# Optimization experiments

Measured on AMD Instinct MI355X. Metric: run time of the kernel, lower is better.

The kernel has to match this reference:

```python
import jax, jax.numpy as jnp
import numpy as np

LAYERS = 3
N_NODES = 100000
N_EDGES = 800000
EMB = 100
EPS = 1e-12  # F.normalize default eps


def setup_inputs() -> dict:
    key = jax.random.key(0)
    ks = jax.random.split(key, 7)
    embedding = jax.random.normal(ks[0], (N_NODES, EMB), dtype=jnp.float32)
    adj_val = jax.random.uniform(ks[1], (N_EDGES,), dtype=jnp.float32)
    w_att = jax.random.normal(ks[2], (EMB, 1), dtype=jnp.float32) * 0.1
    b_att = jax.random.normal(ks[3], (1,), dtype=jnp.float32) * 0.1
    w_items = jax.random.normal(ks[4], (LAYERS, EMB, EMB), dtype=jnp.float32) * 0.1
    adj_row = jax.random.randint(ks[5], (N_EDGES,), 0, N_NODES, dtype=jnp.int32)
    adj_col = jax.random.randint(ks[6], (N_EDGES,), 0, N_NODES, dtype=jnp.int32)
    return {"embedding": embedding, "adj_val": adj_val, "w_att": w_att,
            "b_att": b_att, "w_items": w_items, "adj_row": adj_row, "adj_col": adj_col}


def reference(embedding, adj_val, w_att, b_att, w_items, adj_row, adj_col):
    n = embedding.shape[0]
    # column-degree normalization: adjacency.multiply(1/adjacency.sum(axis=0))
    degree = jax.ops.segment_sum(adj_val, adj_col, num_segments=n)  # [N]
    vals = adj_val / degree[adj_col]  # per-edge normalized value

    x = embedding
    final = embedding
    for i in range(LAYERS):
        scores = x @ w_att + b_att              # [N,1]
        attw = jax.nn.softmax(scores, axis=0)   # softmax over nodes (dim=0)
        x = x @ w_items[i].T                    # nn.Linear (no bias)
        m = x * attw                            # attention-weighted features
        # sparse mm: out[r] = sum_{edges e: row[e]=r} vals[e] * m[col[e]]
        gathered = m[adj_col] * vals[:, None]   # [E, EMB]
        x = jax.ops.segment_sum(gathered, adj_row, num_segments=n)
        # F.normalize(p=2, dim=-1)
        norm = jnp.linalg.norm(x, axis=-1, keepdims=True)
        x = x / jnp.maximum(norm, EPS)
        final = final + x
    return final / (LAYERS + 1)
```

## Files before the change

### kernel.cpp

```cpp
#include <hip/hip_runtime.h>
#include <hip/hip_bf16.h>

#define NN 100000
#define NE 800000
#define EM 100
#define NL 3

typedef short bf16x8 __attribute__((ext_vector_type(8)));
typedef float f32x4  __attribute__((ext_vector_type(4)));

static constexpr size_t OFF_XB   = 0;
static constexpr size_t OFF_M    = OFF_XB   + (size_t)NN*128*2;
static constexpr size_t OFF_F    = OFF_M    + (size_t)NN*128*2;
static constexpr size_t OFF_DEG  = OFF_F    + (size_t)NN*EM*2;
static constexpr size_t OFF_SC   = OFF_DEG  + (size_t)NN*4;
static constexpr size_t OFF_ES   = OFF_SC   + (size_t)NN*4;
static constexpr size_t OFF_CNT  = OFF_ES   + (size_t)NE*8;
static constexpr size_t OFF_RP   = OFF_CNT  + (size_t)NN*4;
static constexpr size_t OFF_CUR  = OFF_RP   + (size_t)(NN+64)*4;
static constexpr size_t OFF_BS   = OFF_CUR  + (size_t)NN*4;
static constexpr size_t OFF_BIN  = OFF_BS   + 512;
static constexpr size_t OFF_FLAG = OFF_BIN  + 16384;
static constexpr size_t OFF_WAT  = OFF_FLAG + 16;
static constexpr size_t OFF_WBF  = OFF_WAT  + 512;

__device__ inline float ldf(const void* p, int i, int f32) {
    return f32 ? ((const float*)p)[i]
               : __bfloat162float(((const __hip_bfloat16*)p)[i]);
}

__device__ inline float bflo(unsigned int u) { return __uint_as_float(u << 16); }
__device__ inline float bfhi(unsigned int u) { return __uint_as_float(u & 0xFFFF0000u); }
__device__ inline unsigned int pack2bf(float a, float b) {
    __hip_bfloat16 ha = __float2bfloat16(a), hb = __float2bfloat16(b);
    unsigned short ua = *(unsigned short*)&ha, ub = *(unsigned short*)&hb;
    return (unsigned int)ua | ((unsigned int)ub << 16);
}

__device__ inline int probe_block(const void* p, int nsamp) {
    __shared__ int sflag;
    int tid = threadIdx.x;
    if (tid < 64) {
        const unsigned short* h = (const unsigned short*)p;
        int big = 0;
        for (int i = tid; i < nsamp; i += 64) {
            int ex = (h[2 * i] >> 7) & 0xFF;
            big += (ex >= 134) ? 1 : 0;
        }
        #pragma unroll
        for (int off = 32; off; off >>= 1) big += __shfl_xor(big, off);
        if (tid == 0) sflag = (big >= 2) ? 1 : 0;
    }
    __syncthreads();
    int f = sflag;
    __syncthreads();
    return f;
}

__global__ __launch_bounds__(256) void k_setup(const void* w_att, const void* w_itm,
                                               float* deg, int* counts, float* bins,
                                               float* wat, unsigned short* wbf) {
    int fw = probe_block(w_att, 50);
    int fi = probe_block(w_itm, 256);
    int i = blockIdx.x * 256 + threadIdx.x;
    if (i < NN) { deg[i] = 0.f; counts[i] = 0; }
    if (i < 4096) bins[i] = 0.f;
    if (i < 128) wat[i] = (i < EM) ? ldf(w_att, i, fw) : 0.f;
    if (i < NL * 112 * 128) {
        int l = i / (112 * 128), rem = i % (112 * 128);
        int n = rem >> 7, k = rem & 127;
        float v = (n < EM && k < EM) ? ldf(w_itm, (l * EM + n) * EM + k, fi) : 0.f;
        __hip_bfloat16 b = __float2bfloat16(v);
        wbf[i] = *(unsigned short*)&b;
    }
}

__global__ __launch_bounds__(256) void k_initxf(const void* __restrict__ emb,
                                                const float* __restrict__ wat,
                                                unsigned int* __restrict__ xbf,
                                                unsigned int* __restrict__ fin,
                                                float* __restrict__ scores, int* flags,
                                                float* __restrict__ bins) {
    __shared__ float sb[4];
    int femb = probe_block(emb, 256);
    if (blockIdx.x == 0 && threadIdx.x == 0) flags[0] = femb;
    int lane = threadIdx.x & 63, w = threadIdx.x >> 6;
    int r = blockIdx.x * 4 + w;
    float f0 = 0.f, f1 = 0.f, part = 0.f;
    bool act = lane < 50;
    if (act) {
        if (femb) {
            float2 t = ((const float2*)emb)[(size_t)r * 50 + lane];
            f0 = t.x; f1 = t.y;
        } else {
            unsigned int u = ((const unsigned int*)emb)[(size_t)r * 50 + lane];
            f0 = bflo(u); f1 = bfhi(u);
        }
        float2 wv = *(const float2*)(wat + 2 * lane);
        part = f0 * wv.x + f1 * wv.y;
        fin[(size_t)r * 50 + lane] = pack2bf(f0, f1);
    }
    xbf[(size_t)r * 64 + lane] = act ? pack2bf(f0, f1) : 0u;
    #pragma unroll
    for (int off = 32; off; off >>= 1) part += __shfl_xor(part, off);
    if (lane == 0) {
        float p = expf(part);
        scores[r] = p;
        sb[w] = p;
    }
    __syncthreads();
    if (threadIdx.x == 0)
        atomicAdd(&bins[blockIdx.x & 1023], sb[0] + sb[1] + sb[2] + sb[3]);
}

__global__ __launch_bounds__(256) void k_deg(const void* __restrict__ val,
                                             const int* __restrict__ row, const int* __restrict__ col,
                                             float* deg, int* counts) {
    int fav = probe_block(val, 256);
    int e = blockIdx.x * 256 + threadIdx.x;
    if (e >= NE) return;
    atomicAdd(&deg[col[e]], ldf(val, e, fav));
    atomicAdd(&counts[row[e]], 1);
}

__global__ __launch_bounds__(256) void k_scanA(const int* __restrict__ counts, int* excl, int* bsum) {
    __shared__ int s[256];
    int base = blockIdx.x * 1024;
    int tid = threadIdx.x;
    int v[4]; int t = 0;
    #pragma unroll
    for (int i = 0; i < 4; i++) {
        int idx = base + tid * 4 + i;
        v[i] = (idx < NN) ? counts[idx] : 0;
        t += v[i];
    }
    s[tid] = t; __syncthreads();
    for (int off = 1; off < 256; off <<= 1) {
        int add = (tid >= off) ? s[tid - off] : 0;
        __syncthreads();
        s[tid] += add;
        __syncthreads();
    }
    int ex = (tid == 0) ? 0 : s[tid - 1];
    #pragma unroll
    for (int i = 0; i < 4; i++) {
        int idx = base + tid * 4 + i;
        if (idx < NN) excl[idx] = ex;
        ex += v[i];
    }
    if (tid == 255) bsum[blockIdx.x] = s[255];
}

__global__ __launch_bounds__(256) void k_scanC(int* rowptr, int* cursor, const int* __restrict__ bsum) {
    __shared__ int spfx;
    int tid = threadIdx.x;
    int gi = blockIdx.x >> 2;
    if (tid < 64) {
        int t = (tid < gi) ? bsum[tid] : 0;
        if (tid + 64 < gi) t += bsum[tid + 64];
        #pragma unroll
        for (int off = 32; off; off >>= 1) t += __shfl_xor(t, off);
        if (tid == 0) spfx = t;
    }
    __syncthreads();
    int pfx = spfx;
    int i = blockIdx.x * 256 + tid;
    if (i < NN) {
        int v = rowptr[i] + pfx;
        rowptr[i] = v; cursor[i] = v;
        if (i == 0) rowptr[NN] = NE;
    }
}

__global__ __launch_bounds__(256) void k_scatter(const int* __restrict__ row, const int* __restrict__ col,
                                                 const void* __restrict__ aval,
                                                 const float* __restrict__ deg, int* cursor,
                                                 int2* es) {
    int fav = probe_block(aval, 256);
    int e = blockIdx.x * 256 + threadIdx.x;
    if (e >= NE) return;
    int r = row[e];
    int c = col[e];
    int pos = atomicAdd(&cursor[r], 1);
    float v = ldf(aval, e, fav) / deg[c];
    es[pos] = make_int2(c, __float_as_int(v));
}

__global__ __launch_bounds__(256) void k_gemm(const unsigned short* __restrict__ xbf,
                                              const unsigned short* __restrict__ wbf,
                                              const float* __restrict__ scores,
                                              const float* __restrict__ bins,
                                              unsigned short* __restrict__ m, int layer) {
    int wid = threadIdx.x >> 6, lane = threadIdx.x & 63;
    int row0 = blockIdx.x * 64 + wid * 16;
    if (row0 >= NN) return;
    int c15 = lane & 15, quad = lane >> 4;

    float bsum = 0.f;
    const f32x4* bp = (const f32x4*)(bins + layer * 1024);
    #pragma unroll
    for (int t = 0; t < 4; t++) {
        f32x4 bv = bp[t * 64 + lane];
        bsum += bv[0] + bv[1] + bv[2] + bv[3];
    }
    #pragma unroll
    for (int off = 32; off; off >>= 1) bsum += __shfl_xor(bsum, off);
    float inv_sum = 1.0f / bsum;

    const bf16x8* xa = (const bf16x8*)(xbf + (size_t)(row0 + c15) * 128 + quad * 8);
    bf16x8 a[4];
    #pragma unroll
    for (int kq = 0; kq < 4; kq++) a[kq] = xa[kq * 4];

    float att[4];
    #pragma unroll
    for (int r = 0; r < 4; r++) att[r] = scores[row0 + quad * 4 + r] * inv_sum;

    const bf16x8* wb = (const bf16x8*)(wbf + (size_t)layer * 112 * 128
                                       + (size_t)c15 * 128 + quad * 8);
    #pragma unroll
    for (int nt = 0; nt < 7; nt++) {
        f32x4 acc = {0.f, 0.f, 0.f, 0.f};
        #pragma unroll
        for (int kq = 0; kq < 4; kq++) {
            bf16x8 b = wb[nt * 256 + kq * 4];
            acc = __builtin_amdgcn_mfma_f32_16x16x32_bf16(a[kq], b, acc, 0, 0, 0);
        }
        int col = nt * 16 + c15;
        #pragma unroll
        for (int r = 0; r < 4; r++) {
            int grow = row0 + quad * 4 + r;
            unsigned short v = 0;
            if (col < EM) {
                __hip_bfloat16 bvv = __float2bfloat16(acc[r] * att[r]);
                v = *(unsigned short*)&bvv;
            }
            m[(size_t)grow * 128 + col] = v;
        }
    }
    #pragma unroll
    for (int r = 0; r < 4; r++) {
        int grow = row0 + quad * 4 + r;
        m[(size_t)grow * 128 + 112 + c15] = 0;
    }
}

__global__ __launch_bounds__(256) void k_spmm(const int* __restrict__ rowptr,
                                              const int2* __restrict__ es,
                                              const unsigned short* __restrict__ m,
                                              const float* __restrict__ wat,
                                              unsigned int* __restrict__ xbf,
                                              unsigned int* __restrict__ fin,
                                              float* __restrict__ scores,
                                              void* __restrict__ out, const int* flags,
                                              float* __restrict__ bins,
                                              int layer, int last) {
    __shared__ float sb[4];
    int lane = threadIdx.x & 63;
    int w = threadIdx.x >> 6;
    int r = blockIdx.x * 4 + w;
    int slot = lane >> 4, k = lane & 15;
    int s = rowptr[r], e = rowptr[r + 1];
    const char* mq = (const char*)m;

    float acc[8] = {0.f, 0.f, 0.f, 0.f, 0.f, 0.f, 0.f, 0.f};
    for (int i = s; i < e; i += 8) {
        int i0 = i + slot, i1 = i + 4 + slot;
        int j0 = i0 < e - 1 ? i0 : e - 1;
        int j1 = i1 < e - 1 ? i1 : e - 1;
        int2 c0 = es[j0];
        int2 c1 = es[j1];
        float v0 = (i0 < e) ? __int_as_float(c0.y) : 0.f;
        float v1 = (i1 < e) ? __int_as_float(c1.y) : 0.f;
        uint4 u0 = *(const uint4*)(mq + (((size_t)c0.x) << 8) + (k << 4));
        uint4 u1 = *(const uint4*)(mq + (((size_t)c1.x) << 8) + (k << 4));
        const unsigned int* p0 = (const unsigned int*)&u0;
        const unsigned int* p1 = (const unsigned int*)&u1;
        #pragma unroll
        for (int t = 0; t < 4; t++) {
            acc[2 * t]     += v0 * bflo(p0[t]);
            acc[2 * t + 1] += v0 * bfhi(p0[t]);
        }
        #pragma unroll
        for (int t = 0; t < 4; t++) {
            acc[2 * t]     += v1 * bflo(p1[t]);
            acc[2 * t + 1] += v1 * bfhi(p1[t]);
        }
    }
    #pragma unroll
    for (int t = 0; t < 8; t++) {
        acc[t] += __shfl_xor(acc[t], 16);
        acc[t] += __shfl_xor(acc[t], 32);
    }
    float sq = 0.f;
    #pragma unroll
    for (int t = 0; t < 8; t++) sq += acc[t] * acc[t];
    #pragma unroll
    for (int off = 8; off; off >>= 1) sq += __shfl_xor(sq, off);
    float rn = 1.f / fmaxf(sqrtf(sq), 1e-12f);
    float n[8];
    #pragma unroll
    for (int t = 0; t < 8; t++) n[t] = acc[t] * rn;

    float part = 0.f;
    if (slot == 0) {
        if (!last) {
            uint4 q;
            q.x = pack2bf(n[0], n[1]); q.y = pack2bf(n[2], n[3]);
            q.z = pack2bf(n[4], n[5]); q.w = pack2bf(n[6], n[7]);
            *(uint4*)(xbf + (size_t)r * 64 + k * 4) = q;
        }
        if (k <= 12) {
            unsigned int fu[4] = {0u, 0u, 0u, 0u};
            size_t fb = (size_t)r * 50 + k * 4;
            uint2 fa = *(const uint2*)(fin + fb);
            fu[0] = fa.x; fu[1] = fa.y;
            if (k < 12) {
                uint2 fbv = *(const uint2*)(fin + fb + 2);
                fu[2] = fbv.x; fu[3] = fbv.y;
            }
            float fn[8];
            #pragma unroll
            for (int t = 0; t < 4; t++) {
                fn[2 * t]     = bflo(fu[t]) + n[2 * t];
                fn[2 * t + 1] = bfhi(fu[t]) + n[2 * t + 1];
            }
            if (!last) {
                uint2 pa, pb;
                pa.x = pack2bf(fn[0], fn[1]); pa.y = pack2bf(fn[2], fn[3]);
                pb.x = pack2bf(fn[4], fn[5]); pb.y = pack2bf(fn[6], fn[7]);
                *(uint2*)(fin + fb) = pa;
                if (k < 12) *(uint2*)(fin + fb + 2) = pb;
                float4 w0 = *(const float4*)(wat + k * 8);
                float4 w1 = *(const float4*)(wat + k * 8 + 4);
                part = n[0] * w0.x + n[1] * w0.y + n[2] * w0.z + n[3] * w0.w
                     + n[4] * w1.x + n[5] * w1.y + n[6] * w1.z + n[7] * w1.w;
            } else {
                if (flags[0]) {
                    float4 A, B;
                    A.x = fn[0] * 0.25f; A.y = fn[1] * 0.25f; A.z = fn[2] * 0.25f; A.w = fn[3] * 0.25f;
                    B.x = fn[4] * 0.25f; B.y = fn[5] * 0.25f; B.z = fn[6] * 0.25f; B.w = fn[7] * 0.25f;
                    float* ob = (float*)out + (size_t)r * 100 + k * 8;
                    *(float4*)ob = A;
                    if (k < 12) *(float4*)(ob + 4) = B;
                } else {
                    uint2 pa, pb;
                    pa.x = pack2bf(fn[0] * 0.25f, fn[1] * 0.25f);
                    pa.y = pack2bf(fn[2] * 0.25f, fn[3] * 0.25f);
                    pb.x = pack2bf(fn[4] * 0.25f, fn[5] * 0.25f);
                    pb.y = pack2bf(fn[6] * 0.25f, fn[7] * 0.25f);
                    unsigned int* ob = (unsigned int*)out + (size_t)r * 50 + k * 4;
                    *(uint2*)ob = pa;
                    if (k < 12) *(uint2*)(ob + 2) = pb;
                }
            }
        }
    }
    if (!last) {
        #pragma unroll
        for (int off = 8; off; off >>= 1) part += __shfl_xor(part, off);
        if (lane == 0) {
            float p = expf(part);
            scores[r] = p;
            sb[w] = p;
        }
        __syncthreads();
        if (threadIdx.x == 0)
            atomicAdd(&bins[(layer + 1) * 1024 + (blockIdx.x & 1023)],
                      sb[0] + sb[1] + sb[2] + sb[3]);
    }
}

extern "C" void kernel_launch(void* const* d_in, const int* in_sizes, int n_in,
                              void* d_out, int out_size, void* d_ws, size_t ws_size,
                              hipStream_t stream) {
    const void* emb   = d_in[0];
    const void* aval  = d_in[1];
    const void* w_att = d_in[2];
    const void* w_itm = d_in[4];
    const int* arow = (const int*)d_in[5];
    const int* acol = (const int*)d_in[6];

    char* w = (char*)d_ws;
    unsigned int*   xbf    = (unsigned int*)(w + OFF_XB);
    unsigned short* m      = (unsigned short*)(w + OFF_M);
    unsigned int*   fin    = (unsigned int*)(w + OFF_F);
    float*          deg    = (float*)(w + OFF_DEG);
    float*          scores = (float*)(w + OFF_SC);
    int2*           es     = (int2*) (w + OFF_ES);
    int*            counts = (int*)  (w + OFF_CNT);
    int*            rowptr = (int*)  (w + OFF_RP);
    int*            cursor = (int*)  (w + OFF_CUR);
    int*            bsum   = (int*)  (w + OFF_BS);
    float*          bins   = (float*)(w + OFF_BIN);
    int*            flags  = (int*)  (w + OFF_FLAG);
    float*          wat    = (float*)(w + OFF_WAT);
    unsigned short* wbf    = (unsigned short*)(w + OFF_WBF);

    const int GN   = (NN + 255) / 256;
    const int GNE  = (NE + 255) / 256;
    const int GSCN = (NN + 1023) / 1024;
    const int GW4  = (NN + 3) / 4;
    const int GGE  = (NN + 63) / 64;

    k_setup<<<GN, 256, 0, stream>>>(w_att, w_itm, deg, counts, bins, wat, wbf);
    k_initxf<<<GW4, 256, 0, stream>>>(emb, wat, xbf, fin, scores, flags, bins);
    k_deg<<<GNE, 256, 0, stream>>>(aval, arow, acol, deg, counts);
    k_scanA<<<GSCN, 256, 0, stream>>>(counts, rowptr, bsum);
    k_scanC<<<GN, 256, 0, stream>>>(rowptr, cursor, bsum);
    k_scatter<<<GNE, 256, 0, stream>>>(arow, acol, aval, deg, cursor, es);

    for (int l = 0; l < NL; l++) {
        k_gemm<<<GGE, 256, 0, stream>>>((const unsigned short*)xbf, wbf, scores, bins, m, l);
        k_spmm<<<GW4, 256, 0, stream>>>(rowptr, es, m, wat, xbf, fin, scores,
                                        d_out, flags, bins, l, (l == NL - 1) ? 1 : 0);
    }
}
```

Measured before the change: 519.0 us.

## Use fixed-point integer atomics for degree and softmax bins; fold inverse degree into GEMM

Degree and softmax-denominator accumulations now use 64-bit fixed-point integer atomics instead of float atomics. This makes the sums deterministic and may avoid float-atomic costs. The per-edge division by column degree moves out of the scatter into the GEMM epilogue, where each row's attention weight is scaled by 1/deg. This removes a random gather of deg per edge, but adds 64-bit atomics, a conversion pass in the scan, and fixed-point quantisation error.

```diff
diff --git a/kernel.cpp b/kernel.cpp
--- a/kernel.cpp
+++ b/kernel.cpp
@@ -8,6 +8,7 @@
 
 typedef short bf16x8 __attribute__((ext_vector_type(8)));
 typedef float f32x4  __attribute__((ext_vector_type(4)));
+typedef unsigned long long u64;
 
 static constexpr size_t OFF_XB   = 0;
 static constexpr size_t OFF_M    = OFF_XB   + (size_t)NN*128*2;
@@ -18,11 +19,17 @@
 static constexpr size_t OFF_CNT  = OFF_ES   + (size_t)NE*8;
 static constexpr size_t OFF_RP   = OFF_CNT  + (size_t)NN*4;
 static constexpr size_t OFF_CUR  = OFF_RP   + (size_t)(NN+64)*4;
-static constexpr size_t OFF_BS   = OFF_CUR  + (size_t)NN*4;
+static constexpr size_t OFF_DGF  = OFF_CUR  + (size_t)NN*4;
+static constexpr size_t OFF_BS   = OFF_DGF  + (size_t)NN*8;
 static constexpr size_t OFF_BIN  = OFF_BS   + 512;
-static constexpr size_t OFF_FLAG = OFF_BIN  + 16384;
+static constexpr size_t OFF_FLAG = OFF_BIN  + 32768;
 static constexpr size_t OFF_WAT  = OFF_FLAG + 16;
 static constexpr size_t OFF_WBF  = OFF_WAT  + 512;
+
+#define DEG_SCALE  4294967296.0f
+#define DEG_INV    (1.0f/4294967296.0f)
+#define BIN_SCALE  1048576.0f
+#define BIN_INV    (1.0f/1048576.0f)
 
 __device__ inline float ldf(const void* p, int i, int f32) {
     return f32 ? ((const float*)p)[i]
@@ -58,13 +65,13 @@
 }
 
 __global__ __launch_bounds__(256) void k_setup(const void* w_att, const void* w_itm,
-                                               float* deg, int* counts, float* bins,
+                                               u64* degfix, int* counts, u64* bins,
                                                float* wat, unsigned short* wbf) {
     int fw = probe_block(w_att, 50);
     int fi = probe_block(w_itm, 256);
     int i = blockIdx.x * 256 + threadIdx.x;
-    if (i < NN) { deg[i] = 0.f; counts[i] = 0; }
-    if (i < 4096) bins[i] = 0.f;
+    if (i < NN) { degfix[i] = 0ull; counts[i] = 0; }
+    if (i < 4096) bins[i] = 0ull;
     if (i < 128) wat[i] = (i < EM) ? ldf(w_att, i, fw) : 0.f;
     if (i < NL * 112 * 128) {
         int l = i / (112 * 128), rem = i % (112 * 128);
@@ -80,7 +87,7 @@
                                                 unsigned int* __restrict__ xbf,
                                                 unsigned int* __restrict__ fin,
                                                 float* __restrict__ scores, int* flags,
-                                                float* __restrict__ bins) {
+                                                u64* __restrict__ bins) {
     __shared__ float sb[4];
     int femb = probe_block(emb, 256);
     if (blockIdx.x == 0 && threadIdx.x == 0) flags[0] = femb;
@@ -109,21 +116,25 @@
         sb[w] = p;
     }
     __syncthreads();
-    if (threadIdx.x == 0)
-        atomicAdd(&bins[blockIdx.x & 1023], sb[0] + sb[1] + sb[2] + sb[3]);
+    if (threadIdx.x == 0) {
+        float t = sb[0] + sb[1] + sb[2] + sb[3];
+        atomicAdd(&bins[blockIdx.x & 1023], (u64)llrintf(t * BIN_SCALE));
+    }
 }
 
 __global__ __launch_bounds__(256) void k_deg(const void* __restrict__ val,
                                              const int* __restrict__ row, const int* __restrict__ col,
-                                             float* deg, int* counts) {
+                                             u64* degfix, int* counts) {
     int fav = probe_block(val, 256);
     int e = blockIdx.x * 256 + threadIdx.x;
     if (e >= NE) return;
-    atomicAdd(&deg[col[e]], ldf(val, e, fav));
+    float v = ldf(val, e, fav);
+    atomicAdd(&degfix[col[e]], (u64)llrintf(v * DEG_SCALE));
     atomicAdd(&counts[row[e]], 1);
 }
 
-__global__ __launch_bounds__(256) void k_scanA(const int* __restrict__ counts, int* excl, int* bsum) {
+__global__ __launch_bounds__(256) void k_scanA(const int* __restrict__ counts, int* excl, int* bsum,
+                                               const u64* __restrict__ degfix, float* __restrict__ deg) {
     __shared__ int s[256];
     int base = blockIdx.x * 1024;
     int tid = threadIdx.x;
@@ -132,6 +143,7 @@
     for (int i = 0; i < 4; i++) {
         int idx = base + tid * 4 + i;
         v[i] = (idx < NN) ? counts[idx] : 0;
+        if (idx < NN) deg[idx] = (float)degfix[idx] * DEG_INV;
         t += v[i];
     }
     s[tid] = t; __syncthreads();
@@ -174,38 +186,34 @@
 
 __global__ __launch_bounds__(256) void k_scatter(const int* __restrict__ row, const int* __restrict__ col,
                                                  const void* __restrict__ aval,
-                                                 const float* __restrict__ deg, int* cursor,
-                                                 int2* es) {
+                                                 int* cursor, int2* es) {
     int fav = probe_block(aval, 256);
     int e = blockIdx.x * 256 + threadIdx.x;
     if (e >= NE) return;
     int r = row[e];
     int c = col[e];
     int pos = atomicAdd(&cursor[r], 1);
-    float v = ldf(aval, e, fav) / deg[c];
-    es[pos] = make_int2(c, __float_as_int(v));
+    es[pos] = make_int2(c, __float_as_int(ldf(aval, e, fav)));
 }
 
 __global__ __launch_bounds__(256) void k_gemm(const unsigned short* __restrict__ xbf,
                                               const unsigned short* __restrict__ wbf,
                                               const float* __restrict__ scores,
-                                              const float* __restrict__ bins,
+                                              const u64* __restrict__ bins,
+                                              const float* __restrict__ deg,
                                               unsigned short* __restrict__ m, int layer) {
     int wid = threadIdx.x >> 6, lane = threadIdx.x & 63;
     int row0 = blockIdx.x * 64 + wid * 16;
     if (row0 >= NN) return;
     int c15 = lane & 15, quad = lane >> 4;
 
-    float bsum = 0.f;
-    const f32x4* bp = (const f32x4*)(bins + layer * 1024);
-    #pragma unroll
-    for (int t = 0; t < 4; t++) {
-        f32x4 bv = bp[t * 64 + lane];
-        bsum += bv[0] + bv[1] + bv[2] + bv[3];
-    }
-    #pragma unroll
-    for (int off = 32; off; off >>= 1) bsum += __shfl_xor(bsum, off);
-    float inv_sum = 1.0f / bsum;
+    u64 bs = 0;
+    const u64* bp = bins + (size_t)layer * 1024;
+    #pragma unroll
+    for (int t = 0; t < 16; t++) bs += bp[t * 64 + lane];
+    #pragma unroll
+    for (int off = 32; off; off >>= 1) bs += __shfl_xor(bs, off);
+    float inv_sum = 1.0f / ((float)bs * BIN_INV);
 
     const bf16x8* xa = (const bf16x8*)(xbf + (size_t)(row0 + c15) * 128 + quad * 8);
     bf16x8 a[4];
@@ -214,7 +222,12 @@
 
     float att[4];
     #pragma unroll
-    for (int r = 0; r < 4; r++) att[r] = scores[row0 + quad * 4 + r] * inv_sum;
+    for (int r = 0; r < 4; r++) {
+        int grow = row0 + quad * 4 + r;
+        float dv = deg[grow];
+        float invd = dv > 0.f ? 1.0f / dv : 0.f;
+        att[r] = scores[grow] * inv_sum * invd;
+    }
 
     const bf16x8* wb = (const bf16x8*)(wbf + (size_t)layer * 112 * 128
                                        + (size_t)c15 * 128 + quad * 8);
@@ -253,7 +266,7 @@
                                               unsigned int* __restrict__ fin,
                                               float* __restrict__ scores,
                                               void* __restrict__ out, const int* flags,
-                                              float* __restrict__ bins,
+                                              u64* __restrict__ bins,
                                               int layer, int last) {
     __shared__ float sb[4];
     int lane = threadIdx.x & 63;
@@ -365,9 +378,11 @@
             sb[w] = p;
         }
         __syncthreads();
-        if (threadIdx.x == 0)
-            atomicAdd(&bins[(layer + 1) * 1024 + (blockIdx.x & 1023)],
-                      sb[0] + sb[1] + sb[2] + sb[3]);
+        if (threadIdx.x == 0) {
+            float t = sb[0] + sb[1] + sb[2] + sb[3];
+            atomicAdd(&bins[(size_t)(layer + 1) * 1024 + (blockIdx.x & 1023)],
+                      (u64)llrintf(t * BIN_SCALE));
+        }
     }
 }
 
@@ -391,8 +406,9 @@
     int*            counts = (int*)  (w + OFF_CNT);
     int*            rowptr = (int*)  (w + OFF_RP);
     int*            cursor = (int*)  (w + OFF_CUR);
+    u64*            degfix = (u64*)  (w + OFF_DGF);
     int*            bsum   = (int*)  (w + OFF_BS);
-    float*          bins   = (float*)(w + OFF_BIN);
+    u64*            bins   = (u64*)  (w + OFF_BIN);
     int*            flags  = (int*)  (w + OFF_FLAG);
     float*          wat    = (float*)(w + OFF_WAT);
     unsigned short* wbf    = (unsigned short*)(w + OFF_WBF);
@@ -403,15 +419,15 @@
     const int GW4  = (NN + 3) / 4;
     const int GGE  = (NN + 63) / 64;
 
-    k_setup<<<GN, 256, 0, stream>>>(w_att, w_itm, deg, counts, bins, wat, wbf);
+    k_setup<<<GN, 256, 0, stream>>>(w_att, w_itm, degfix, counts, bins, wat, wbf);
     k_initxf<<<GW4, 256, 0, stream>>>(emb, wat, xbf, fin, scores, flags, bins);
-    k_deg<<<GNE, 256, 0, stream>>>(aval, arow, acol, deg, counts);
-    k_scanA<<<GSCN, 256, 0, stream>>>(counts, rowptr, bsum);
+    k_deg<<<GNE, 256, 0, stream>>>(aval, arow, acol, degfix, counts);
+    k_scanA<<<GSCN, 256, 0, stream>>>(counts, rowptr, bsum, degfix, deg);
     k_scanC<<<GN, 256, 0, stream>>>(rowptr, cursor, bsum);
-    k_scatter<<<GNE, 256, 0, stream>>>(arow, acol, aval, deg, cursor, es);
+    k_scatter<<<GNE, 256, 0, stream>>>(arow, acol, aval, cursor, es);
 
     for (int l = 0; l < NL; l++) {
-        k_gemm<<<GGE, 256, 0, stream>>>((const unsigned short*)xbf, wbf, scores, bins, m, l);
+        k_gemm<<<GGE, 256, 0, stream>>>((const unsigned short*)xbf, wbf, scores, bins, deg, m, l);
         k_spmm<<<GW4, 256, 0, stream>>>(rowptr, es, m, wat, xbf, fin, scores,
                                         d_out, flags, bins, l, (l == NL - 1) ? 1 : 0);
     }
```

Result: no change. 518.0 us (-0.2%).
